# Performance work log

Measured on AMD Instinct MI355X. Metric: run time of the kernel, lower is better.

Reference implementation:

```python
import jax, jax.numpy as jnp
import numpy as np

H = 100  # hidden size

def _lstm_layer(x, Wih, Whh, b):
    # x: [B, T, D_in]; Wih: [4H, D_in]; Whh: [4H, H]; b: [4H]
    # Precompute input contribution for all timesteps (batched GEMM).
    xw = jnp.einsum('btd,gd->btg', x, Wih) + b            # [B, T, 4H]
    B = x.shape[0]
    h0 = jnp.zeros((B, H), x.dtype)
    c0 = jnp.zeros((B, H), x.dtype)
    WhhT = Whh.T                                          # [H, 4H]

    def step(carry, xw_t):
        h, c = carry
        gates = xw_t + h @ WhhT                           # [B, 4H]
        i, f, g, o = jnp.split(gates, 4, axis=-1)         # PyTorch order i,f,g,o
        i = jax.nn.sigmoid(i)
        f = jax.nn.sigmoid(f)
        g = jnp.tanh(g)
        o = jax.nn.sigmoid(o)
        c = f * c + i * g
        h = o * jnp.tanh(c)
        return (h, c), h

    _, hs = jax.lax.scan(step, (h0, c0), jnp.swapaxes(xw, 0, 1))  # [T, B, H]
    return jnp.swapaxes(hs, 0, 1)                         # [B, T, H]


def setup_inputs() -> dict:
    key = jax.random.key(0)
    ks = jax.random.split(key, 12)
    B, T = 512, 512
    s = 0.08  # small init scale to avoid gate saturation
    return {
        'z':    jax.random.normal(ks[0], (B, T, 1), jnp.float32),
        'Wih0': jax.random.normal(ks[1], (4 * H, 1), jnp.float32) * s,
        'Whh0': jax.random.normal(ks[2], (4 * H, H), jnp.float32) * s,
        'b0':   jax.random.normal(ks[3], (4 * H,), jnp.float32) * s,
        'Wih1': jax.random.normal(ks[4], (4 * H, H), jnp.float32) * s,
        'Whh1': jax.random.normal(ks[5], (4 * H, H), jnp.float32) * s,
        'b1':   jax.random.normal(ks[6], (4 * H,), jnp.float32) * s,
        'Wih2': jax.random.normal(ks[7], (4 * H, H), jnp.float32) * s,
        'Whh2': jax.random.normal(ks[8], (4 * H, H), jnp.float32) * s,
        'b2':   jax.random.normal(ks[9], (4 * H,), jnp.float32) * s,
        'Wp':   jax.random.normal(ks[10], (1, H), jnp.float32) * s,
        'bp':   jax.random.normal(ks[11], (1,), jnp.float32) * s,
    }


def reference(z, Wih0, Whh0, b0, Wih1, Whh1, b1, Wih2, Whh2, b2, Wp, bp):
    h = _lstm_layer(z, Wih0, Whh0, b0)
    h = _lstm_layer(h, Wih1, Whh1, b1)
    h = _lstm_layer(h, Wih2, Whh2, b2)       # [B, T, H]
    return jnp.tanh(jnp.einsum('bth,oh->bto', h, Wp) + bp)  # [B, T, 1]
```

## Files before the change

kernel.cpp:

```cpp
#include <hip/hip_runtime.h>
#include <cstdint>
#include <cstddef>


#define HH 100
#define G4 400
#define NB 512
#define NT 512
#define WSTR 448
#define MT 64
#define NTL 64
#define NNT 7

#define PIN44 __attribute__((amdgpu_flat_work_group_size(512, 512), \
                             amdgpu_waves_per_eu(4, 4)))
#define PIN22 __attribute__((amdgpu_flat_work_group_size(512, 512), \
                             amdgpu_waves_per_eu(2, 2)))

__device__ __forceinline__ float sigm(float x) {
  return 1.0f / (1.0f + __expf(-x));
}
__device__ __forceinline__ float tanh_(float x) {
  return 1.0f - 2.0f / (__expf(2.0f * x) + 1.0f);
}
__device__ __forceinline__ float qb1(float v) {
  return __int_as_float(__builtin_amdgcn_ds_swizzle(__float_as_int(v), 0x8055));
}
__device__ __forceinline__ float qb2(float v) {
  return __int_as_float(__builtin_amdgcn_ds_swizzle(__float_as_int(v), 0x80AA));
}
__device__ __forceinline__ float qb3(float v) {
  return __int_as_float(__builtin_amdgcn_ds_swizzle(__float_as_int(v), 0x80FF));
}

__global__ __launch_bounds__(256) void wprep(
    const float* __restrict__ Wih,
    const float* __restrict__ bias,
    float* __restrict__ wT,
    float* __restrict__ bp)
{
  int idx = blockIdx.x * blockDim.x + threadIdx.x;
  if (idx >= HH * WSTR) return;
  int k = idx / WSTR, n = idx % WSTR;
  float v = 0.0f;
  if (n < G4) {
    int row = (n & 3) * HH + (n >> 2);
    v = Wih[(size_t)row * HH + k];
  }
  wT[idx] = v;
  if (idx < WSTR) bp[idx] = (idx < G4) ? bias[(idx & 3) * HH + (idx >> 2)] : 0.0f;
}

__global__ __launch_bounds__(256) void xw_gemm(
    const float* __restrict__ hsrc,
    const float* __restrict__ wT,
    const float* __restrict__ bperm,
    float* __restrict__ xw,
    int t0, int CT)
{
  const int mt = blockIdx.x / NNT, nt = blockIdx.x % NNT;
  const int m0 = mt * MT;
  const int b = m0 / CT, tr0 = m0 % CT;
  const int n0 = nt * NTL;
  const int tid = threadIdx.x;
  const int tx = tid & 15, ty = tid >> 4;

  __shared__ float Asub[HH][MT];
  __shared__ float Bsub[HH][NTL];

  for (int id = tid; id < MT * (HH / 4); id += 256) {
    const int k4 = id / MT, i = id % MT;
    const float4 v = *reinterpret_cast<const float4*>(
        hsrc + ((size_t)b * NT + (t0 + tr0 + i)) * HH + 4 * k4);
    Asub[4 * k4 + 0][i] = v.x;
    Asub[4 * k4 + 1][i] = v.y;
    Asub[4 * k4 + 2][i] = v.z;
    Asub[4 * k4 + 3][i] = v.w;
  }
  for (int id = tid; id < HH * (NTL / 4); id += 256) {
    const int k = id / (NTL / 4), q = id % (NTL / 4);
    const float4 v = *reinterpret_cast<const float4*>(wT + (size_t)k * WSTR + n0 + 4 * q);
    *reinterpret_cast<float4*>(&Bsub[k][4 * q]) = v;
  }
  __syncthreads();

  float acc[4][4] = {};
#pragma unroll 4
  for (int k = 0; k < HH; ++k) {
    const float4 a = *reinterpret_cast<const float4*>(&Asub[k][4 * ty]);
    const float4 bq = *reinterpret_cast<const float4*>(&Bsub[k][4 * tx]);
    acc[0][0] += a.x * bq.x; acc[0][1] += a.x * bq.y; acc[0][2] += a.x * bq.z; acc[0][3] += a.x * bq.w;
    acc[1][0] += a.y * bq.x; acc[1][1] += a.y * bq.y; acc[1][2] += a.y * bq.z; acc[1][3] += a.y * bq.w;
    acc[2][0] += a.z * bq.x; acc[2][1] += a.z * bq.y; acc[2][2] += a.z * bq.z; acc[2][3] += a.z * bq.w;
    acc[3][0] += a.w * bq.x; acc[3][1] += a.w * bq.y; acc[3][2] += a.w * bq.z; acc[3][3] += a.w * bq.w;
  }

  const int n = n0 + 4 * tx;
  if (n + 3 < G4) {
    const float4 bpq = *reinterpret_cast<const float4*>(bperm + n);
#pragma unroll
    for (int jr = 0; jr < 4; ++jr) {
      float4 o;
      o.x = acc[jr][0] + bpq.x; o.y = acc[jr][1] + bpq.y;
      o.z = acc[jr][2] + bpq.z; o.w = acc[jr][3] + bpq.w;
      *reinterpret_cast<float4*>(
          &xw[((size_t)b * CT + tr0 + 4 * ty + jr) * G4 + n]) = o;
    }
  }
}

template <int MODE>
__global__ PIN44 void lstm_rec(
    const float* __restrict__ xsrc,
    const float* __restrict__ Wih,
    const float* __restrict__ Whh,
    const float* __restrict__ bias,
    float* __restrict__ hseq,
    float* __restrict__ cbuf,
    int t0, int tlen)
{
  const int b = blockIdx.x;
  const int tid = threadIdx.x;

  __shared__ __align__(16) float h_lds[2][HH];

  const bool isG = tid < G4;
  const int u = tid >> 2, g = tid & 3;
  const int row = g * HH + u;

  float w[HH];
  float bb = 0.f, c = 0.f, wih1 = 0.f;
  if (isG) {
    const float4* w4 = reinterpret_cast<const float4*>(Whh + (size_t)row * HH);
#pragma unroll
    for (int k = 0; k < HH / 4; ++k) {
      float4 v = w4[k];
      w[4 * k] = v.x; w[4 * k + 1] = v.y; w[4 * k + 2] = v.z; w[4 * k + 3] = v.w;
    }
    if constexpr (MODE == 1) {
      wih1 = Wih[row];
      bb = bias[row];
    }
  }

  if (t0 == 0) {
    if (tid < HH) h_lds[0][tid] = 0.0f;
  } else {
    if (tid < HH) h_lds[0][tid] = hseq[((size_t)b * NT + (t0 - 1)) * HH + tid];
    if (isG && g == 0) c = cbuf[b * HH + u];
  }

  const float* xwp = xsrc + (size_t)b * tlen * G4 + tid;
  const float* zp  = xsrc + (size_t)b * NT + t0;
  float* hp = hseq + ((size_t)b * NT + t0) * HH;

  float xa_n = 0.f, zc = 0.f;
  if constexpr (MODE == 0) {
    if (isG) xa_n = *xwp;
  } else {
    zc = *zp;
  }
  __syncthreads();

  for (int s = 0; s < tlen; ++s) {
    const int cur = s & 1, nxt = cur ^ 1;

    float xa = 0.f, zn = 0.f;
    if constexpr (MODE == 0) {
      xa = xa_n;
      xwp += (s + 1 < tlen) ? G4 : 0;
      if (isG) xa_n = *xwp;
    } else {
      zp += (s + 1 < tlen) ? 1 : 0;
      zn = *zp;
    }

    if (isG) {
      float a0 = 0.f, a1 = 0.f, a2 = 0.f, a3 = 0.f;
      const float4* h4 = reinterpret_cast<const float4*>(h_lds[cur]);
#pragma unroll
      for (int k = 0; k < HH / 4; ++k) {
        float4 v = h4[k];
        a0 += v.x * w[4 * k];     a1 += v.y * w[4 * k + 1];
        a2 += v.z * w[4 * k + 2]; a3 += v.w * w[4 * k + 3];
      }
      float acc = xa + ((a0 + a1) + (a2 + a3));
      if constexpr (MODE == 1) acc += bb + wih1 * zc;
      float act = (g == 2) ? tanh_(acc) : sigm(acc);
      float fv = qb1(act);
      float gv = qb2(act);
      float ov = qb3(act);
      if (g == 0) {
        c = fv * c + act * gv;
        float hv = ov * tanh_(c);
        h_lds[nxt][u] = hv;
        hp[u] = hv;
      }
    }
    hp += HH;
    if constexpr (MODE == 1) zc = zn;
    __syncthreads();
  }

  if (isG && g == 0) cbuf[b * HH + u] = c;
}

__global__ PIN22 void lstm_fused(
    const float* x,
    const float* __restrict__ Wih,
    const float* __restrict__ Whh,
    const float* __restrict__ bias,
    float* hseq)
{
  const int b = blockIdx.x;
  const int tid = threadIdx.x;
  __shared__ __align__(16) float h_dbuf[2][HH];
  __shared__ __align__(16) float x_dbuf[2][HH];
  const bool isG = tid < G4;
  const int u = tid >> 2, g = tid & 3;
  const int row = g * HH + u;
  float whh[HH], wih[HH];
  float bb = 0.f, c = 0.f;
  if (isG) {
    const float4* wh4 = reinterpret_cast<const float4*>(Whh + (size_t)row * HH);
    const float4* wi4 = reinterpret_cast<const float4*>(Wih + (size_t)row * HH);
#pragma unroll
    for (int k = 0; k < HH / 4; ++k) {
      float4 a = wh4[k];
      whh[4 * k] = a.x; whh[4 * k + 1] = a.y; whh[4 * k + 2] = a.z; whh[4 * k + 3] = a.w;
      float4 bq = wi4[k];
      wih[4 * k] = bq.x; wih[4 * k + 1] = bq.y; wih[4 * k + 2] = bq.z; wih[4 * k + 3] = bq.w;
    }
    bb = bias[row];
  }
  if (tid < HH) h_dbuf[0][tid] = 0.0f;
  const float* xb = x + (size_t)b * NT * HH;
  float* hb = hseq + (size_t)b * NT * HH;
  const unsigned pf = (unsigned)(tid - 448);
  if (pf < 25u)
    reinterpret_cast<float4*>(x_dbuf[0])[pf] = reinterpret_cast<const float4*>(xb)[pf];
  __syncthreads();
  for (int t = 0; t < NT; ++t) {
    const int cur = t & 1, nxt = cur ^ 1;
    if (pf < 25u) {
      int tt = (t + 1 < NT) ? t + 1 : NT - 1;
      reinterpret_cast<float4*>(x_dbuf[nxt])[pf] =
          reinterpret_cast<const float4*>(xb + (size_t)tt * HH)[pf];
    }
    if (isG) {
      float a0 = 0.f, a1 = 0.f, a2 = 0.f, a3 = 0.f;
      const float4* x4 = reinterpret_cast<const float4*>(x_dbuf[cur]);
      const float4* h4 = reinterpret_cast<const float4*>(h_dbuf[cur]);
#pragma unroll
      for (int k = 0; k < HH / 4; ++k) {
        float4 v = x4[k];
        a0 += v.x * wih[4 * k];     a1 += v.y * wih[4 * k + 1];
        a2 += v.z * wih[4 * k + 2]; a3 += v.w * wih[4 * k + 3];
      }
#pragma unroll
      for (int k = 0; k < HH / 4; ++k) {
        float4 v = h4[k];
        a0 += v.x * whh[4 * k];     a1 += v.y * whh[4 * k + 1];
        a2 += v.z * whh[4 * k + 2]; a3 += v.w * whh[4 * k + 3];
      }
      float acc = bb + ((a0 + a1) + (a2 + a3));
      float act = (g == 2) ? tanh_(acc) : sigm(acc);
      float fv = qb1(act);
      float gv = qb2(act);
      float ov = qb3(act);
      if (g == 0) {
        c = fv * c + act * gv;
        float hv = ov * tanh_(c);
        h_dbuf[nxt][u] = hv;
        hb[(size_t)t * HH + u] = hv;
      }
    }
    __syncthreads();
  }
}

__global__ __launch_bounds__(256) void proj_kernel(
    const float* __restrict__ hseq,
    const float* __restrict__ Wp,
    const float* __restrict__ bp,
    float* __restrict__ out)
{
  int idx = blockIdx.x * blockDim.x + threadIdx.x;
  if (idx >= NB * NT) return;
  const float4* h4 = reinterpret_cast<const float4*>(hseq + (size_t)idx * HH);
  const float4* w4 = reinterpret_cast<const float4*>(Wp);
  float a0 = 0.f, a1 = 0.f, a2 = 0.f, a3 = 0.f;
#pragma unroll
  for (int k = 0; k < HH / 4; ++k) {
    float4 h = h4[k];
    float4 w = w4[k];
    a0 += h.x * w.x; a1 += h.y * w.y; a2 += h.z * w.z; a3 += h.w * w.w;
  }
  out[idx] = tanh_(((a0 + a1) + (a2 + a3)) + bp[0]);
}

extern "C" void kernel_launch(void* const* d_in, const int* in_sizes, int n_in,
                              void* d_out, int out_size, void* d_ws, size_t ws_size,
                              hipStream_t stream) {
  const float* z    = (const float*)d_in[0];
  const float* Wih0 = (const float*)d_in[1];
  const float* Whh0 = (const float*)d_in[2];
  const float* b0   = (const float*)d_in[3];
  const float* Wih1 = (const float*)d_in[4];
  const float* Whh1 = (const float*)d_in[5];
  const float* b1   = (const float*)d_in[6];
  const float* Wih2 = (const float*)d_in[7];
  const float* Whh2 = (const float*)d_in[8];
  const float* b2   = (const float*)d_in[9];
  const float* Wp   = (const float*)d_in[10];
  const float* bp   = (const float*)d_in[11];
  float* out = (float*)d_out;

  float* hbuf = (float*)d_ws;
  float* cbuf = hbuf + (size_t)NB * NT * HH;
  float* wt1  = cbuf + (size_t)NB * HH;
  float* wt2  = wt1 + (size_t)HH * WSTR;
  float* bp1  = wt2 + (size_t)HH * WSTR;
  float* bp2  = bp1 + WSTR;
  float* xwb  = bp2 + WSTR;

  const size_t fixed = (size_t)(bp2 + WSTR - hbuf) * 4;
  int CT = 0;
  for (int c : {128, 64}) {
    if (fixed + (size_t)NB * c * G4 * 4 <= ws_size) { CT = c; break; }
  }

  lstm_rec<1><<<NB, 512, 0, stream>>>(z, Wih0, Whh0, b0, hbuf, cbuf, 0, NT);

  if (CT > 0) {
    wprep<<<(HH * WSTR + 255) / 256, 256, 0, stream>>>(Wih1, b1, wt1, bp1);
    wprep<<<(HH * WSTR + 255) / 256, 256, 0, stream>>>(Wih2, b2, wt2, bp2);
    const float* wtL[2] = {wt1, wt2};
    const float* bpL[2] = {bp1, bp2};
    const float* WhhL[2] = {Whh1, Whh2};
    const int gemm_grid = (NB * CT / MT) * NNT;
    for (int l = 0; l < 2; ++l) {
      for (int t0 = 0; t0 < NT; t0 += CT) {
        xw_gemm<<<gemm_grid, 256, 0, stream>>>(hbuf, wtL[l], bpL[l], xwb, t0, CT);
        lstm_rec<0><<<NB, 512, 0, stream>>>(xwb, nullptr, WhhL[l], nullptr,
                                            hbuf, cbuf, t0, CT);
      }
    }
  } else {
    lstm_fused<<<NB, 512, 0, stream>>>(hbuf, Wih1, Whh1, b1, hbuf);
    lstm_fused<<<NB, 512, 0, stream>>>(hbuf, Wih2, Whh2, b2, hbuf);
  }

  proj_kernel<<<(NB * NT + 255) / 256, 256, 0, stream>>>(hbuf, Wp, bp, out);
}
```

Before: 2.701 ms.

## Split recurrent weights between registers and LDS, offload loads/stores to spare waves

Rewrites the recurrent LSTM kernels so each gate thread keeps 88 of its 100 Whh weights in registers and reads the last 12 from an LDS tail array. This lowers register pressure under the 4-waves-per-EU pin and avoids spills. Global traffic moves to the otherwise idle threads 448+: they prefetch the next timestep's xw or z into double-buffered LDS and write the previous h row to global with float4 stores. The gate threads then only do LDS reads and math, at the cost of extra LDS traffic and a fixed 128-step chunk size with no fallback size of 64.

```diff
diff --git a/kernel.cpp b/kernel.cpp
--- a/kernel.cpp
+++ b/kernel.cpp
@@ -7,6 +7,9 @@
 #define G4 400
 #define NB 512
 #define NT 512
+#define TLEN 128
+#define KREG 88
+#define KTL 12
 #define WSTR 448
 #define MT 64
 #define NTL 64
@@ -31,6 +34,188 @@
 }
 __device__ __forceinline__ float qb3(float v) {
   return __int_as_float(__builtin_amdgcn_ds_swizzle(__float_as_int(v), 0x80FF));
+}
+
+__device__ __forceinline__ float gate_dot(const float* __restrict__ hbuf_lds,
+                                          const float w[KREG],
+                                          volatile const float* wt) {
+  const float4* h4 = reinterpret_cast<const float4*>(hbuf_lds);
+  float a0 = 0.f, a1 = 0.f, a2 = 0.f, a3 = 0.f;
+#pragma unroll
+  for (int k = 0; k < KREG / 4; ++k) {
+    float4 v = h4[k];
+    a0 += v.x * w[4 * k];     a1 += v.y * w[4 * k + 1];
+    a2 += v.z * w[4 * k + 2]; a3 += v.w * w[4 * k + 3];
+  }
+  float4 t0 = h4[22], t1 = h4[23], t2 = h4[24];
+  a0 += t0.x * wt[0 * G4];  a1 += t0.y * wt[1 * G4];
+  a2 += t0.z * wt[2 * G4];  a3 += t0.w * wt[3 * G4];
+  a0 += t1.x * wt[4 * G4];  a1 += t1.y * wt[5 * G4];
+  a2 += t1.z * wt[6 * G4];  a3 += t1.w * wt[7 * G4];
+  a0 += t2.x * wt[8 * G4];  a1 += t2.y * wt[9 * G4];
+  a2 += t2.z * wt[10 * G4]; a3 += t2.w * wt[11 * G4];
+  return (a0 + a1) + (a2 + a3);
+}
+
+__global__ PIN44 void rec0(
+    const float* __restrict__ z,
+    const float* __restrict__ Wih,
+    const float* __restrict__ Whh,
+    const float* __restrict__ bias,
+    float* __restrict__ hseq)
+{
+  const int b = blockIdx.x;
+  const int tid = threadIdx.x;
+
+  __shared__ __align__(16) float h_lds[2][HH];
+  __shared__ __align__(16) float z_lds[2];
+  __shared__ __align__(16) float wtail[KTL][G4];
+
+  const bool isG = tid < G4;
+  const int u = tid >> 2, g = tid & 3;
+  const int row = g * HH + u;
+
+  float w[KREG];
+  float bb = 0.f, wih1 = 0.f, c = 0.f;
+  if (isG) {
+    const float4* w4 = reinterpret_cast<const float4*>(Whh + (size_t)row * HH);
+#pragma unroll
+    for (int k = 0; k < KREG / 4; ++k) {
+      float4 v = w4[k];
+      w[4 * k] = v.x; w[4 * k + 1] = v.y; w[4 * k + 2] = v.z; w[4 * k + 3] = v.w;
+    }
+#pragma unroll
+    for (int j = 0; j < KTL; ++j)
+      wtail[j][tid] = Whh[(size_t)row * HH + KREG + j];
+    wih1 = Wih[row];
+    bb = bias[row];
+  }
+  if (tid < HH) h_lds[0][tid] = 0.0f;
+
+  const float* zb = z + (size_t)b * NT;
+  float* hb = hseq + (size_t)b * NT * HH;
+  if (tid == 448) z_lds[0] = zb[0];
+  volatile const float* wt = &wtail[0][0] + tid;
+  __syncthreads();
+
+  for (int s = 0; s < NT; ++s) {
+    const int cur = s & 1, nxt = cur ^ 1;
+    if (isG) {
+      float zc = z_lds[cur];
+      float acc = bb + wih1 * zc + gate_dot(h_lds[cur], w, wt);
+      float act = (g == 2) ? tanh_(acc) : sigm(acc);
+      float fv = qb1(act);
+      float gv = qb2(act);
+      float ov = qb3(act);
+      if (g == 0) {
+        c = fv * c + act * gv;
+        h_lds[nxt][u] = ov * tanh_(c);
+      }
+    } else if (tid >= 448) {
+      const int q = tid - 448;
+      if (q == 0) {
+        int sn = (s + 1 < NT) ? s + 1 : NT - 1;
+        z_lds[nxt] = zb[sn];
+      }
+      if (q < 25 && s > 0) {
+        reinterpret_cast<float4*>(hb + (size_t)(s - 1) * HH)[q] =
+            reinterpret_cast<const float4*>(h_lds[cur])[q];
+      }
+    }
+    __syncthreads();
+  }
+  if (tid >= 448 && tid < 448 + 25) {
+    reinterpret_cast<float4*>(hb + (size_t)(NT - 1) * HH)[tid - 448] =
+        reinterpret_cast<const float4*>(h_lds[0])[tid - 448];
+  }
+}
+
+__global__ PIN44 void recx(
+    const float* __restrict__ xw,
+    const float* __restrict__ Whh,
+    float* __restrict__ hseq,
+    float* __restrict__ cbuf,
+    int t0)
+{
+  const int b = blockIdx.x;
+  const int tid = threadIdx.x;
+
+  __shared__ __align__(16) float h_lds[2][HH];
+  __shared__ __align__(16) float xw_lds[2][G4];
+  __shared__ __align__(16) float wtail[KTL][G4];
+
+  const bool isG = tid < G4;
+  const int u = tid >> 2, g = tid & 3;
+  const int row = g * HH + u;
+
+  float w[KREG];
+  float c = 0.f;
+  if (isG) {
+    const float4* w4 = reinterpret_cast<const float4*>(Whh + (size_t)row * HH);
+#pragma unroll
+    for (int k = 0; k < KREG / 4; ++k) {
+      float4 v = w4[k];
+      w[4 * k] = v.x; w[4 * k + 1] = v.y; w[4 * k + 2] = v.z; w[4 * k + 3] = v.w;
+    }
+#pragma unroll
+    for (int j = 0; j < KTL; ++j)
+      wtail[j][tid] = Whh[(size_t)row * HH + KREG + j];
+  }
+
+  if (t0 == 0) {
+    if (tid < HH) h_lds[0][tid] = 0.0f;
+  } else {
+    if (tid < 25)
+      reinterpret_cast<float4*>(h_lds[0])[tid] =
+          reinterpret_cast<const float4*>(
+              hseq + ((size_t)b * NT + (t0 - 1)) * HH)[tid];
+    if (isG && g == 0) c = cbuf[b * HH + u];
+  }
+
+  const float* xwb = xw + (size_t)b * TLEN * G4;
+  float* hb = hseq + ((size_t)b * NT + t0) * HH;
+
+  if (tid >= 448) {
+    const int q = tid - 448;
+    const float4* x4 = reinterpret_cast<const float4*>(xwb);
+    if (q < 100) reinterpret_cast<float4*>(xw_lds[0])[q] = x4[q];
+    const int q2 = q + 64;
+    if (q2 < 100) reinterpret_cast<float4*>(xw_lds[0])[q2] = x4[q2];
+  }
+  volatile const float* wt = &wtail[0][0] + tid;
+  __syncthreads();
+
+  for (int s = 0; s < TLEN; ++s) {
+    const int cur = s & 1, nxt = cur ^ 1;
+    if (isG) {
+      float acc = xw_lds[cur][tid] + gate_dot(h_lds[cur], w, wt);
+      float act = (g == 2) ? tanh_(acc) : sigm(acc);
+      float fv = qb1(act);
+      float gv = qb2(act);
+      float ov = qb3(act);
+      if (g == 0) {
+        c = fv * c + act * gv;
+        h_lds[nxt][u] = ov * tanh_(c);
+      }
+    } else if (tid >= 448) {
+      const int q = tid - 448;
+      const int sn = (s + 1 < TLEN) ? s + 1 : TLEN - 1;
+      const float4* x4 = reinterpret_cast<const float4*>(xwb + (size_t)sn * G4);
+      if (q < 100) reinterpret_cast<float4*>(xw_lds[nxt])[q] = x4[q];
+      const int q2 = q + 64;
+      if (q2 < 100) reinterpret_cast<float4*>(xw_lds[nxt])[q2] = x4[q2];
+      if (q < 25 && (s + t0 > 0)) {
+        reinterpret_cast<float4*>(hb + (size_t)(s - 1) * HH)[q] =
+            reinterpret_cast<const float4*>(h_lds[cur])[q];
+      }
+    }
+    __syncthreads();
+  }
+  if (isG && g == 0) cbuf[b * HH + u] = c;
+  if (tid >= 448 && tid < 448 + 25) {
+    reinterpret_cast<float4*>(hb + (size_t)(TLEN - 1) * HH)[tid - 448] =
+        reinterpret_cast<const float4*>(h_lds[0])[tid - 448];
+  }
 }
 
 __global__ __launch_bounds__(256) void wprep(
@@ -56,11 +241,11 @@
     const float* __restrict__ wT,
     const float* __restrict__ bperm,
     float* __restrict__ xw,
-    int t0, int CT)
+    int t0)
 {
   const int mt = blockIdx.x / NNT, nt = blockIdx.x % NNT;
   const int m0 = mt * MT;
-  const int b = m0 / CT, tr0 = m0 % CT;
+  const int b = m0 / TLEN, tr0 = m0 % TLEN;
   const int n0 = nt * NTL;
   const int tid = threadIdx.x;
   const int tx = tid & 15, ty = tid >> 4;
@@ -104,105 +289,9 @@
       o.x = acc[jr][0] + bpq.x; o.y = acc[jr][1] + bpq.y;
       o.z = acc[jr][2] + bpq.z; o.w = acc[jr][3] + bpq.w;
       *reinterpret_cast<float4*>(
-          &xw[((size_t)b * CT + tr0 + 4 * ty + jr) * G4 + n]) = o;
-    }
-  }
-}
-
-template <int MODE>
-__global__ PIN44 void lstm_rec(
-    const float* __restrict__ xsrc,
-    const float* __restrict__ Wih,
-    const float* __restrict__ Whh,
-    const float* __restrict__ bias,
-    float* __restrict__ hseq,
-    float* __restrict__ cbuf,
-    int t0, int tlen)
-{
-  const int b = blockIdx.x;
-  const int tid = threadIdx.x;
-
-  __shared__ __align__(16) float h_lds[2][HH];
-
-  const bool isG = tid < G4;
-  const int u = tid >> 2, g = tid & 3;
-  const int row = g * HH + u;
-
-  float w[HH];
-  float bb = 0.f, c = 0.f, wih1 = 0.f;
-  if (isG) {
-    const float4* w4 = reinterpret_cast<const float4*>(Whh + (size_t)row * HH);
-#pragma unroll
-    for (int k = 0; k < HH / 4; ++k) {
-      float4 v = w4[k];
-      w[4 * k] = v.x; w[4 * k + 1] = v.y; w[4 * k + 2] = v.z; w[4 * k + 3] = v.w;
-    }
-    if constexpr (MODE == 1) {
-      wih1 = Wih[row];
-      bb = bias[row];
-    }
-  }
-
-  if (t0 == 0) {
-    if (tid < HH) h_lds[0][tid] = 0.0f;
-  } else {
-    if (tid < HH) h_lds[0][tid] = hseq[((size_t)b * NT + (t0 - 1)) * HH + tid];
-    if (isG && g == 0) c = cbuf[b * HH + u];
-  }
-
-  const float* xwp = xsrc + (size_t)b * tlen * G4 + tid;
-  const float* zp  = xsrc + (size_t)b * NT + t0;
-  float* hp = hseq + ((size_t)b * NT + t0) * HH;
-
-  float xa_n = 0.f, zc = 0.f;
-  if constexpr (MODE == 0) {
-    if (isG) xa_n = *xwp;
-  } else {
-    zc = *zp;
-  }
-  __syncthreads();
-
-  for (int s = 0; s < tlen; ++s) {
-    const int cur = s & 1, nxt = cur ^ 1;
-
-    float xa = 0.f, zn = 0.f;
-    if constexpr (MODE == 0) {
-      xa = xa_n;
-      xwp += (s + 1 < tlen) ? G4 : 0;
-      if (isG) xa_n = *xwp;
-    } else {
-      zp += (s + 1 < tlen) ? 1 : 0;
-      zn = *zp;
-    }
-
-    if (isG) {
-      float a0 = 0.f, a1 = 0.f, a2 = 0.f, a3 = 0.f;
-      const float4* h4 = reinterpret_cast<const float4*>(h_lds[cur]);
-#pragma unroll
-      for (int k = 0; k < HH / 4; ++k) {
-        float4 v = h4[k];
-        a0 += v.x * w[4 * k];     a1 += v.y * w[4 * k + 1];
-        a2 += v.z * w[4 * k + 2]; a3 += v.w * w[4 * k + 3];
-      }
-      float acc = xa + ((a0 + a1) + (a2 + a3));
-      if constexpr (MODE == 1) acc += bb + wih1 * zc;
-      float act = (g == 2) ? tanh_(acc) : sigm(acc);
-      float fv = qb1(act);
-      float gv = qb2(act);
-      float ov = qb3(act);
-      if (g == 0) {
-        c = fv * c + act * gv;
-        float hv = ov * tanh_(c);
-        h_lds[nxt][u] = hv;
-        hp[u] = hv;
-      }
-    }
-    hp += HH;
-    if constexpr (MODE == 1) zc = zn;
-    __syncthreads();
-  }
-
-  if (isG && g == 0) cbuf[b * HH + u] = c;
+          &xw[((size_t)b * TLEN + tr0 + 4 * ty + jr) * G4 + n]) = o;
+    }
+  }
 }
 
 __global__ PIN22 void lstm_fused(
@@ -324,26 +413,21 @@
   float* bp2  = bp1 + WSTR;
   float* xwb  = bp2 + WSTR;
 
-  const size_t fixed = (size_t)(bp2 + WSTR - hbuf) * 4;
-  int CT = 0;
-  for (int c : {128, 64}) {
-    if (fixed + (size_t)NB * c * G4 * 4 <= ws_size) { CT = c; break; }
-  }
-
-  lstm_rec<1><<<NB, 512, 0, stream>>>(z, Wih0, Whh0, b0, hbuf, cbuf, 0, NT);
-
-  if (CT > 0) {
+  const size_t need = ((size_t)(bp2 + WSTR - hbuf) + (size_t)NB * TLEN * G4) * 4;
+
+  rec0<<<NB, 512, 0, stream>>>(z, Wih0, Whh0, b0, hbuf);
+
+  if (need <= ws_size) {
     wprep<<<(HH * WSTR + 255) / 256, 256, 0, stream>>>(Wih1, b1, wt1, bp1);
     wprep<<<(HH * WSTR + 255) / 256, 256, 0, stream>>>(Wih2, b2, wt2, bp2);
     const float* wtL[2] = {wt1, wt2};
     const float* bpL[2] = {bp1, bp2};
     const float* WhhL[2] = {Whh1, Whh2};
-    const int gemm_grid = (NB * CT / MT) * NNT;
+    const int gemm_grid = (NB * TLEN / MT) * NNT;
     for (int l = 0; l < 2; ++l) {
-      for (int t0 = 0; t0 < NT; t0 += CT) {
-        xw_gemm<<<gemm_grid, 256, 0, stream>>>(hbuf, wtL[l], bpL[l], xwb, t0, CT);
-        lstm_rec<0><<<NB, 512, 0, stream>>>(xwb, nullptr, WhhL[l], nullptr,
-                                            hbuf, cbuf, t0, CT);
+      for (int t0 = 0; t0 < NT; t0 += TLEN) {
+        xw_gemm<<<gemm_grid, 256, 0, stream>>>(hbuf, wtL[l], bpL[l], xwb, t0);
+        recx<<<NB, 512, 0, stream>>>(xwb, WhhL[l], hbuf, cbuf, t0);
       }
     }
   } else {
```

Measured after the change: 4.137 ms. 1.53x slower.
